# Kernel optimization log

Hardware: AMD Instinct MI355X
Metric: run time of the kernel (lower is better)

## Reference

```python
import jax, jax.numpy as jnp
import numpy as np

SOBEL_X = jnp.array([[-1., 0., 1.], [-2., 0., 2.], [-1., 0., 1.]], dtype=jnp.float32)
SOBEL_Y = jnp.array([[-1., -2., -1.], [0., 0., 0.], [1., 2., 1.]], dtype=jnp.float32)


def _depthwise_sobel(x, k2d):
    # x: [N, 3, H, W]; k2d: [3,3] -> depthwise kernel [3,1,3,3] (OIHW, groups=3)
    kern = jnp.broadcast_to(k2d, (3, 1, 3, 3)).astype(x.dtype)
    return jax.lax.conv_general_dilated(
        x, kern, window_strides=(1, 1), padding=((1, 1), (1, 1)),
        dimension_numbers=('NCHW', 'OIHW', 'NCHW'), feature_group_count=3)


def _edge_map(x):
    ex = _depthwise_sobel(x, SOBEL_X)
    ey = _depthwise_sobel(x, SOBEL_Y)
    return jnp.sqrt(ex * ex + ey * ey + 1e-6)


def setup_inputs() -> dict:
    key = jax.random.key(0)
    k1, k2 = jax.random.split(key)
    shape = (2, 8, 3, 512, 512)  # [B, T, C, H, W]
    pred = jax.random.uniform(k1, shape, dtype=jnp.float32)
    target = jax.random.uniform(k2, shape, dtype=jnp.float32)
    return {"pred": pred, "target": target}


def reference(pred, target):
    if pred.ndim == 5:
        B, T, C, H, W = pred.shape
        pred = pred.reshape(B * T, C, H, W)
        target = target.reshape(B * T, C, H, W)
    pred_edge = _edge_map(pred)
    target_edge = _edge_map(target)
    return jnp.mean(jnp.abs(pred_edge - target_edge))
```

## Files before the change

kernel.cpp:

```cpp
#include <hip/hip_runtime.h>


#define EW 512
#define EH 512
#define EPLANE (EH * EW)
#define NPLANES 48
#define TOTAL_PX (NPLANES * EPLANE)
#define ROWS_PT 8
#define THREADS_TOTAL (TOTAL_PX / (4 * ROWS_PT))
#define BLOCKS_MAIN (THREADS_TOTAL / 256)

__device__ __forceinline__ void load_row6(float* a, const float* __restrict__ row,
                                          int x0, bool valid) {
    if (valid) {
        float4 c = *reinterpret_cast<const float4*>(row + x0);
        a[1] = c.x; a[2] = c.y; a[3] = c.z; a[4] = c.w;
        a[0] = (x0 > 0)      ? row[x0 - 1] : 0.f;
        a[5] = (x0 + 4 < EW) ? row[x0 + 4] : 0.f;
    } else {
        a[0] = a[1] = a[2] = a[3] = a[4] = a[5] = 0.f;
    }
}

__global__ __launch_bounds__(256) void edge_main(const float* __restrict__ pred,
                                                 const float* __restrict__ tgt,
                                                 float* __restrict__ partial) {
    const int t = blockIdx.x * 256 + threadIdx.x;
    const int plane = t >> 13;
    const int s = t & 8191;
    const int y0 = ((s >> 7) & 63) << 3;
    const int x0 = (s & 127) << 2;

    const float* __restrict__ prow = pred + plane * EPLANE + y0 * EW;
    const float* __restrict__ qrow = tgt  + plane * EPLANE + y0 * EW;

    float P[4][6], T[4][6];
    load_row6(P[0], prow - EW, x0, y0 > 0);
    load_row6(T[0], qrow - EW, x0, y0 > 0);
    load_row6(P[1], prow,      x0, true);
    load_row6(T[1], qrow,      x0, true);
    load_row6(P[2], prow + EW, x0, true);
    load_row6(T[2], qrow + EW, x0, true);

    float sum = 0.f;
#pragma unroll
    for (int r = 0; r < ROWS_PT; ++r) {
        if (r < ROWS_PT - 1) {
            const bool v = (y0 + r + 2) < EH;
            load_row6(P[(r + 3) & 3], prow + (r + 2) * EW, x0, v);
            load_row6(T[(r + 3) & 3], qrow + (r + 2) * EW, x0, v);
        }
        float (&Pt)[6] = P[r & 3];
        float (&Pm)[6] = P[(r + 1) & 3];
        float (&Pb)[6] = P[(r + 2) & 3];
        float (&Tt)[6] = T[r & 3];
        float (&Tm)[6] = T[(r + 1) & 3];
        float (&Tb)[6] = T[(r + 2) & 3];
#pragma unroll
        for (int i = 0; i < 4; ++i) {
            float gxp = (Pt[i+2] - Pt[i]) + 2.f * (Pm[i+2] - Pm[i]) + (Pb[i+2] - Pb[i]);
            float gyp = (Pb[i] - Pt[i]) + 2.f * (Pb[i+1] - Pt[i+1]) + (Pb[i+2] - Pt[i+2]);
            float ep  = __builtin_amdgcn_sqrtf(gxp * gxp + gyp * gyp + 1e-6f);
            float gxt = (Tt[i+2] - Tt[i]) + 2.f * (Tm[i+2] - Tm[i]) + (Tb[i+2] - Tb[i]);
            float gyt = (Tb[i] - Tt[i]) + 2.f * (Tb[i+1] - Tt[i+1]) + (Tb[i+2] - Tt[i+2]);
            float et  = __builtin_amdgcn_sqrtf(gxt * gxt + gyt * gyt + 1e-6f);
            sum += fabsf(ep - et);
        }
    }

    for (int off = 32; off > 0; off >>= 1)
        sum += __shfl_down(sum, off, 64);

    __shared__ float wsum[4];
    const int lane = threadIdx.x & 63;
    const int wid  = threadIdx.x >> 6;
    if (lane == 0) wsum[wid] = sum;
    __syncthreads();
    if (threadIdx.x == 0)
        partial[blockIdx.x] = wsum[0] + wsum[1] + wsum[2] + wsum[3];
}

__global__ __launch_bounds__(256) void edge_final(const float* __restrict__ partial,
                                                  int n, float* __restrict__ out) {
    double s = 0.0;
    for (int i = threadIdx.x; i < n; i += 256) s += (double)partial[i];
    __shared__ double sd[256];
    sd[threadIdx.x] = s;
    __syncthreads();
    for (int k = 128; k > 0; k >>= 1) {
        if (threadIdx.x < k) sd[threadIdx.x] += sd[threadIdx.x + k];
        __syncthreads();
    }
    if (threadIdx.x == 0) out[0] = (float)(sd[0] / (double)TOTAL_PX);
}

extern "C" void kernel_launch(void* const* d_in, const int* in_sizes, int n_in,
                              void* d_out, int out_size, void* d_ws, size_t ws_size,
                              hipStream_t stream) {
    const float* pred = (const float*)d_in[0];
    const float* tgt  = (const float*)d_in[1];
    float* partial = (float*)d_ws;
    float* out = (float*)d_out;

    edge_main<<<BLOCKS_MAIN, 256, 0, stream>>>(pred, tgt, partial);
    edge_final<<<1, 256, 0, stream>>>(partial, BLOCKS_MAIN, out);
}
```

Measured before the change: 121.2 us.

## Map one wave per row band, 8 pixels per lane, halo via shuffles

Each wavefront now covers a full 512-wide row band, with each lane handling 8 contiguous columns loaded as two float4s. The left and right halo pixels come from neighbouring lanes through DPP-style shuffles instead of scalar global loads, which removes the unaligned per-thread halo reads. The change also adds a launch-bounds occupancy hint. In exchange it adds 12 shuffles per row and uses more registers per thread, with fewer threads covering the same work.

```diff
diff --git a/kernel.cpp b/kernel.cpp
--- a/kernel.cpp
+++ b/kernel.cpp
@@ -7,63 +7,89 @@
 #define NPLANES 48
 #define TOTAL_PX (NPLANES * EPLANE)
 #define ROWS_PT 8
-#define THREADS_TOTAL (TOTAL_PX / (4 * ROWS_PT))
-#define BLOCKS_MAIN (THREADS_TOTAL / 256)
+#define BANDS (EH / ROWS_PT)
+#define NWAVES (NPLANES * BANDS)
+#define BLOCKS_MAIN (NWAVES / 4)
 
-__device__ __forceinline__ void load_row6(float* a, const float* __restrict__ row,
-                                          int x0, bool valid) {
+__device__ __forceinline__ void load_row8(float* a, const float* __restrict__ p,
+                                          bool valid) {
     if (valid) {
-        float4 c = *reinterpret_cast<const float4*>(row + x0);
-        a[1] = c.x; a[2] = c.y; a[3] = c.z; a[4] = c.w;
-        a[0] = (x0 > 0)      ? row[x0 - 1] : 0.f;
-        a[5] = (x0 + 4 < EW) ? row[x0 + 4] : 0.f;
+        float4 c0 = *reinterpret_cast<const float4*>(p);
+        float4 c1 = *reinterpret_cast<const float4*>(p + 4);
+        a[0] = c0.x; a[1] = c0.y; a[2] = c0.z; a[3] = c0.w;
+        a[4] = c1.x; a[5] = c1.y; a[6] = c1.z; a[7] = c1.w;
     } else {
-        a[0] = a[1] = a[2] = a[3] = a[4] = a[5] = 0.f;
+        a[0] = a[1] = a[2] = a[3] = a[4] = a[5] = a[6] = a[7] = 0.f;
     }
 }
 
-__global__ __launch_bounds__(256) void edge_main(const float* __restrict__ pred,
-                                                 const float* __restrict__ tgt,
-                                                 float* __restrict__ partial) {
-    const int t = blockIdx.x * 256 + threadIdx.x;
-    const int plane = t >> 13;
-    const int s = t & 8191;
-    const int y0 = ((s >> 7) & 63) << 3;
-    const int x0 = (s & 127) << 2;
+#define EXT(arr, l, r, j) ((j) < 0 ? (l) : ((j) > 7 ? (r) : (arr)[(j) < 0 ? 0 : ((j) > 7 ? 7 : (j))]))
 
-    const float* __restrict__ prow = pred + plane * EPLANE + y0 * EW;
-    const float* __restrict__ qrow = tgt  + plane * EPLANE + y0 * EW;
+__global__ __launch_bounds__(256, 4) void edge_main(const float* __restrict__ pred,
+                                                    const float* __restrict__ tgt,
+                                                    float* __restrict__ partial) {
+    const int lane = threadIdx.x & 63;
+    const int w = blockIdx.x * 4 + (threadIdx.x >> 6);
+    const int plane = w >> 6;
+    const int band = w & 63;
+    const int y0 = band << 3;
+    const int x0 = lane << 3;
 
-    float P[4][6], T[4][6];
-    load_row6(P[0], prow - EW, x0, y0 > 0);
-    load_row6(T[0], qrow - EW, x0, y0 > 0);
-    load_row6(P[1], prow,      x0, true);
-    load_row6(T[1], qrow,      x0, true);
-    load_row6(P[2], prow + EW, x0, true);
-    load_row6(T[2], qrow + EW, x0, true);
+    const float* __restrict__ pbase = pred + plane * EPLANE + y0 * EW + x0;
+    const float* __restrict__ qbase = tgt  + plane * EPLANE + y0 * EW + x0;
+
+    float P[4][8], T[4][8];
+    load_row8(P[0], pbase - EW, band > 0);
+    load_row8(T[0], qbase - EW, band > 0);
+    load_row8(P[1], pbase,      true);
+    load_row8(T[1], qbase,      true);
+    load_row8(P[2], pbase + EW, true);
+    load_row8(T[2], qbase + EW, true);
 
     float sum = 0.f;
 #pragma unroll
     for (int r = 0; r < ROWS_PT; ++r) {
         if (r < ROWS_PT - 1) {
             const bool v = (y0 + r + 2) < EH;
-            load_row6(P[(r + 3) & 3], prow + (r + 2) * EW, x0, v);
-            load_row6(T[(r + 3) & 3], qrow + (r + 2) * EW, x0, v);
+            load_row8(P[(r + 3) & 3], pbase + (r + 2) * EW, v);
+            load_row8(T[(r + 3) & 3], qbase + (r + 2) * EW, v);
         }
-        float (&Pt)[6] = P[r & 3];
-        float (&Pm)[6] = P[(r + 1) & 3];
-        float (&Pb)[6] = P[(r + 2) & 3];
-        float (&Tt)[6] = T[r & 3];
-        float (&Tm)[6] = T[(r + 1) & 3];
-        float (&Tb)[6] = T[(r + 2) & 3];
+        float (&Pt)[8] = P[r & 3];
+        float (&Pm)[8] = P[(r + 1) & 3];
+        float (&Pb)[8] = P[(r + 2) & 3];
+        float (&Tt)[8] = T[r & 3];
+        float (&Tm)[8] = T[(r + 1) & 3];
+        float (&Tb)[8] = T[(r + 2) & 3];
+
+        float ptl = __shfl_up(Pt[7], 1);  ptl = lane ? ptl : 0.f;
+        float pml = __shfl_up(Pm[7], 1);  pml = lane ? pml : 0.f;
+        float pbl = __shfl_up(Pb[7], 1);  pbl = lane ? pbl : 0.f;
+        float ttl = __shfl_up(Tt[7], 1);  ttl = lane ? ttl : 0.f;
+        float tml = __shfl_up(Tm[7], 1);  tml = lane ? tml : 0.f;
+        float tbl = __shfl_up(Tb[7], 1);  tbl = lane ? tbl : 0.f;
+        float ptr_ = __shfl_down(Pt[0], 1);  ptr_ = (lane < 63) ? ptr_ : 0.f;
+        float pmr = __shfl_down(Pm[0], 1);   pmr  = (lane < 63) ? pmr  : 0.f;
+        float pbr = __shfl_down(Pb[0], 1);   pbr  = (lane < 63) ? pbr  : 0.f;
+        float ttr = __shfl_down(Tt[0], 1);   ttr  = (lane < 63) ? ttr  : 0.f;
+        float tmr = __shfl_down(Tm[0], 1);   tmr  = (lane < 63) ? tmr  : 0.f;
+        float tbr = __shfl_down(Tb[0], 1);   tbr  = (lane < 63) ? tbr  : 0.f;
+
 #pragma unroll
-        for (int i = 0; i < 4; ++i) {
-            float gxp = (Pt[i+2] - Pt[i]) + 2.f * (Pm[i+2] - Pm[i]) + (Pb[i+2] - Pb[i]);
-            float gyp = (Pb[i] - Pt[i]) + 2.f * (Pb[i+1] - Pt[i+1]) + (Pb[i+2] - Pt[i+2]);
+        for (int i = 0; i < 8; ++i) {
+            float pt_m = EXT(Pt, ptl, ptr_, i - 1), pt_p = EXT(Pt, ptl, ptr_, i + 1);
+            float pm_m = EXT(Pm, pml, pmr, i - 1),  pm_p = EXT(Pm, pml, pmr, i + 1);
+            float pb_m = EXT(Pb, pbl, pbr, i - 1),  pb_p = EXT(Pb, pbl, pbr, i + 1);
+            float gxp = (pt_p - pt_m) + 2.f * (pm_p - pm_m) + (pb_p - pb_m);
+            float gyp = (pb_m - pt_m) + 2.f * (Pb[i] - Pt[i]) + (pb_p - pt_p);
             float ep  = __builtin_amdgcn_sqrtf(gxp * gxp + gyp * gyp + 1e-6f);
-            float gxt = (Tt[i+2] - Tt[i]) + 2.f * (Tm[i+2] - Tm[i]) + (Tb[i+2] - Tb[i]);
-            float gyt = (Tb[i] - Tt[i]) + 2.f * (Tb[i+1] - Tt[i+1]) + (Tb[i+2] - Tt[i+2]);
+
+            float tt_m = EXT(Tt, ttl, ttr, i - 1), tt_p = EXT(Tt, ttl, ttr, i + 1);
+            float tm_m = EXT(Tm, tml, tmr, i - 1), tm_p = EXT(Tm, tml, tmr, i + 1);
+            float tb_m = EXT(Tb, tbl, tbr, i - 1), tb_p = EXT(Tb, tbl, tbr, i + 1);
+            float gxt = (tt_p - tt_m) + 2.f * (tm_p - tm_m) + (tb_p - tb_m);
+            float gyt = (tb_m - tt_m) + 2.f * (Tb[i] - Tt[i]) + (tb_p - tt_p);
             float et  = __builtin_amdgcn_sqrtf(gxt * gxt + gyt * gyt + 1e-6f);
+
             sum += fabsf(ep - et);
         }
     }
@@ -72,8 +98,7 @@
         sum += __shfl_down(sum, off, 64);
 
     __shared__ float wsum[4];
-    const int lane = threadIdx.x & 63;
-    const int wid  = threadIdx.x >> 6;
+    const int wid = threadIdx.x >> 6;
     if (lane == 0) wsum[wid] = sum;
     __syncthreads();
     if (threadIdx.x == 0)
```

After: 162.4 us. 34.0% more time.
